# Kernel optimization log

Measured on AMD Instinct MI355X. Metric: run time of the kernel, lower is better.

Reference implementation:

```python
import jax, jax.numpy as jnp
import numpy as np

B, T, H = 32, 4096, 256
MAX_SENTS = 256  # static upper bound on sentences per doc (doc 0 has exactly 256)


def setup_inputs() -> dict:
    key = jax.random.key(0)
    hie_ins = jax.random.normal(key, (B, T, H), dtype=jnp.float32)
    # Deterministic boundary pattern: doc b has a sentence boundary (token id 1)
    # every (16 + b) tokens; all other tokens get a non-boundary id (2).
    pos = np.arange(T)
    rows = [np.where((pos + 1) % (16 + b) == 0, 1, 2) for b in range(B)]
    batch_x = jnp.asarray(np.stack(rows), dtype=jnp.int32)
    return {"hie_ins": hie_ins, "batch_x": batch_x}


def reference(hie_ins, batch_x):
    # Faithful vectorized version of HieLayer.forward with mean pooling:
    # tokens are assigned to sentence segments by exclusive cumsum of boundary
    # flags; tokens after the last boundary are dropped (as in the torch slicing
    # up to the last cut). Each sentence is mean-pooled over its true length;
    # docs are padded with zeros to MAX_SENTS sentences (== max(doc_lens)).
    _, t, _ = hie_ins.shape
    is_b = (batch_x == 1).astype(jnp.int32)          # (B, T) boundary flags
    sent_id = jnp.cumsum(is_b, axis=1) - is_b        # exclusive cumsum: sentence index per token
    doc_lens = jnp.sum(is_b, axis=1)                 # (B,) number of sentences per doc
    valid = sent_id < doc_lens[:, None]              # drop tokens past last boundary
    seg = jnp.where(valid, sent_id, MAX_SENTS)       # invalid tokens -> overflow bucket

    def per_doc(x, s):
        sums = jax.ops.segment_sum(x, s, num_segments=MAX_SENTS + 1)              # (S+1, H)
        cnts = jax.ops.segment_sum(jnp.ones((t,), x.dtype), s, num_segments=MAX_SENTS + 1)
        return sums[:MAX_SENTS], cnts[:MAX_SENTS]

    sums, cnts = jax.vmap(per_doc)(hie_ins, seg)     # (B, S, H), (B, S)
    pooled = sums / jnp.maximum(cnts, 1.0)[..., None]
    sent_valid = jnp.arange(MAX_SENTS)[None, :] < doc_lens[:, None]
    pooled = jnp.where(sent_valid[..., None], pooled, 0.0)  # zero-pad like F.pad
    return pooled, doc_lens
```

## Files before the change

### kernel.cpp

```cpp
#include <hip/hip_runtime.h>
#include <hip/hip_bf16.h>

#define NB 32
#define NT 4096
#define NH 256
#define NS 256

__global__ void hie_fused_kernel(const float* __restrict__ x,
                                 const int* __restrict__ batch_x,
                                 float* __restrict__ out) {
    const int b    = blockIdx.y;
    const int tid  = threadIdx.x;
    const int wid  = tid >> 6;
    const int lane = tid & 63;

    __shared__ int sm_w[5];
    __shared__ int sm_bpos[NS + 1];
    __shared__ int sm_len;

    const int  base = tid * 16;
    const int4* rp  = reinterpret_cast<const int4*>(batch_x + (size_t)b * NT + base);
    int flags = 0, cnt = 0;
#pragma unroll
    for (int i = 0; i < 4; ++i) {
        int4 v = rp[i];
        int f0 = (v.x == 1), f1 = (v.y == 1), f2 = (v.z == 1), f3 = (v.w == 1);
        flags |= (f0 << (4 * i)) | (f1 << (4 * i + 1)) | (f2 << (4 * i + 2)) | (f3 << (4 * i + 3));
        cnt   += f0 + f1 + f2 + f3;
    }

    int inc = cnt;
#pragma unroll
    for (int off = 1; off < 64; off <<= 1) {
        int u = __shfl_up(inc, off, 64);
        if (lane >= off) inc += u;
    }
    if (lane == 63) sm_w[wid] = inc;
    __syncthreads();
    if (tid == 0) {
        int run = 0;
#pragma unroll
        for (int w = 0; w < 4; ++w) { int t = sm_w[w]; sm_w[w] = run; run += t; }
        sm_w[4]    = run;
        sm_len     = run > NS ? NS : run;
        sm_bpos[0] = -1;
    }
    __syncthreads();

    int idx = (inc - cnt) + sm_w[wid];
#pragma unroll
    for (int i = 0; i < 16; ++i) {
        if ((flags >> i) & 1) {
            if (idx < NS) sm_bpos[idx + 1] = base + i;
            ++idx;
        }
    }
    __syncthreads();

    if (blockIdx.x == 0 && tid == 0)
        out[(size_t)NB * NS * NH + b] = (float)sm_w[4];

    const int s = blockIdx.x * 4 + wid;
    float* o = out + ((size_t)b * NS + s) * NH + lane * 4;

    if (s >= sm_len) {
        *reinterpret_cast<float4*>(o) = make_float4(0.f, 0.f, 0.f, 0.f);
        return;
    }

    const int end   = sm_bpos[s + 1];
    const int start = sm_bpos[s] + 1;
    const int n     = end - start + 1;

    const float4* p = reinterpret_cast<const float4*>(
                          x + ((size_t)b * NT + start) * NH) + lane;
    float4 a0 = make_float4(0.f, 0.f, 0.f, 0.f);
    float4 a1 = make_float4(0.f, 0.f, 0.f, 0.f);
    int k = 0;
    for (; k + 2 <= n; k += 2) {
        float4 v0 = p[0];
        float4 v1 = p[NH / 4];
        a0.x += v0.x; a0.y += v0.y; a0.z += v0.z; a0.w += v0.w;
        a1.x += v1.x; a1.y += v1.y; a1.z += v1.z; a1.w += v1.w;
        p += 2 * (NH / 4);
    }
    if (k < n) {
        float4 v0 = p[0];
        a0.x += v0.x; a0.y += v0.y; a0.z += v0.z; a0.w += v0.w;
    }
    const float inv = 1.0f / (float)n;
    *reinterpret_cast<float4*>(o) = make_float4((a0.x + a1.x) * inv,
                                                (a0.y + a1.y) * inv,
                                                (a0.z + a1.z) * inv,
                                                (a0.w + a1.w) * inv);
}

extern "C" void kernel_launch(void* const* d_in, const int* in_sizes, int n_in,
                              void* d_out, int out_size, void* d_ws, size_t ws_size,
                              hipStream_t stream) {
    const float* hie_ins = (const float*)d_in[0];
    const int*   batch_x = (const int*)d_in[1];
    float*       out     = (float*)d_out;

    hie_fused_kernel<<<dim3(NS / 4, NB), dim3(256), 0, stream>>>(hie_ins, batch_x, out);
}
```

Measured before the change: 29.45 us.

## Split boundary scan into separate kernel and pool each sentence with a full block

The fused kernel, which recomputed the boundary scan in every block, becomes two kernels. The first computes sentence boundary positions and document lengths once per document into workspace. The second pools each sentence with a 256-thread block whose four waves interleave rows and combine partial sums through shared memory. This removes redundant scan work and spreads long sentences across more waves for memory parallelism. In exchange it adds a second launch, a global round trip for the boundaries, and a shared-memory reduction.

```diff
diff --git a/kernel.cpp b/kernel.cpp
--- a/kernel.cpp
+++ b/kernel.cpp
@@ -6,17 +6,16 @@
 #define NH 256
 #define NS 256
 
-__global__ void hie_fused_kernel(const float* __restrict__ x,
-                                 const int* __restrict__ batch_x,
-                                 float* __restrict__ out) {
-    const int b    = blockIdx.y;
+__global__ void hie_scan_kernel(const int* __restrict__ batch_x,
+                                int* __restrict__ bpos,
+                                int* __restrict__ dlen,
+                                float* __restrict__ dout) {
+    const int b    = blockIdx.x;
     const int tid  = threadIdx.x;
     const int wid  = tid >> 6;
     const int lane = tid & 63;
 
     __shared__ int sm_w[5];
-    __shared__ int sm_bpos[NS + 1];
-    __shared__ int sm_len;
 
     const int  base = tid * 16;
     const int4* rp  = reinterpret_cast<const int4*>(batch_x + (size_t)b * NT + base);
@@ -41,9 +40,10 @@
         int run = 0;
 #pragma unroll
         for (int w = 0; w < 4; ++w) { int t = sm_w[w]; sm_w[w] = run; run += t; }
-        sm_w[4]    = run;
-        sm_len     = run > NS ? NS : run;
-        sm_bpos[0] = -1;
+        sm_w[4] = run;
+        bpos[b * (NS + 1)] = -1;
+        dlen[b] = run > NS ? NS : run;
+        dout[(size_t)NB * NS * NH + b] = (float)run;
     }
     __syncthreads();
 
@@ -51,48 +51,60 @@
 #pragma unroll
     for (int i = 0; i < 16; ++i) {
         if ((flags >> i) & 1) {
-            if (idx < NS) sm_bpos[idx + 1] = base + i;
+            if (idx < NS) bpos[b * (NS + 1) + 1 + idx] = base + i;
             ++idx;
         }
     }
-    __syncthreads();
+}
 
-    if (blockIdx.x == 0 && tid == 0)
-        out[(size_t)NB * NS * NH + b] = (float)sm_w[4];
+__global__ void hie_pool_kernel(const float* __restrict__ x,
+                                const int* __restrict__ bpos,
+                                const int* __restrict__ dlen,
+                                float* __restrict__ out) {
+    const int b    = blockIdx.y;
+    const int s    = blockIdx.x;
+    const int tid  = threadIdx.x;
+    const int wid  = tid >> 6;
+    const int lane = tid & 63;
 
-    const int s = blockIdx.x * 4 + wid;
-    float* o = out + ((size_t)b * NS + s) * NH + lane * 4;
+    float* orow = out + ((size_t)b * NS + s) * NH;
 
-    if (s >= sm_len) {
-        *reinterpret_cast<float4*>(o) = make_float4(0.f, 0.f, 0.f, 0.f);
+    const int L = dlen[b];
+    if (s >= L) {
+        orow[tid] = 0.0f;
         return;
     }
 
-    const int end   = sm_bpos[s + 1];
-    const int start = sm_bpos[s] + 1;
+    const int start = bpos[b * (NS + 1) + s] + 1;
+    const int end   = bpos[b * (NS + 1) + s + 1];
     const int n     = end - start + 1;
 
     const float4* p = reinterpret_cast<const float4*>(
-                          x + ((size_t)b * NT + start) * NH) + lane;
+                          x + ((size_t)b * NT + start + wid) * NH) + lane;
+    const int myrows = (n - wid + 3) >> 2;
     float4 a0 = make_float4(0.f, 0.f, 0.f, 0.f);
     float4 a1 = make_float4(0.f, 0.f, 0.f, 0.f);
     int k = 0;
-    for (; k + 2 <= n; k += 2) {
+    for (; k + 2 <= myrows; k += 2) {
         float4 v0 = p[0];
-        float4 v1 = p[NH / 4];
+        float4 v1 = p[4 * (NH / 4)];
         a0.x += v0.x; a0.y += v0.y; a0.z += v0.z; a0.w += v0.w;
         a1.x += v1.x; a1.y += v1.y; a1.z += v1.z; a1.w += v1.w;
-        p += 2 * (NH / 4);
+        p += 8 * (NH / 4);
     }
-    if (k < n) {
+    if (k < myrows) {
         float4 v0 = p[0];
         a0.x += v0.x; a0.y += v0.y; a0.z += v0.z; a0.w += v0.w;
     }
-    const float inv = 1.0f / (float)n;
-    *reinterpret_cast<float4*>(o) = make_float4((a0.x + a1.x) * inv,
-                                                (a0.y + a1.y) * inv,
-                                                (a0.z + a1.z) * inv,
-                                                (a0.w + a1.w) * inv);
+    a0.x += a1.x; a0.y += a1.y; a0.z += a1.z; a0.w += a1.w;
+
+    __shared__ float4 smp[4][64];
+    smp[wid][lane] = a0;
+    __syncthreads();
+
+    const float* smf = reinterpret_cast<const float*>(smp);
+    float v = smf[tid] + smf[256 + tid] + smf[512 + tid] + smf[768 + tid];
+    orow[tid] = v * (1.0f / (float)n);
 }
 
 extern "C" void kernel_launch(void* const* d_in, const int* in_sizes, int n_in,
@@ -102,5 +114,9 @@
     const int*   batch_x = (const int*)d_in[1];
     float*       out     = (float*)d_out;
 
-    hie_fused_kernel<<<dim3(NS / 4, NB), dim3(256), 0, stream>>>(hie_ins, batch_x, out);
+    int* bpos = (int*)d_ws;
+    int* dlen = bpos + NB * (NS + 1);
+
+    hie_scan_kernel<<<dim3(NB), dim3(256), 0, stream>>>(batch_x, bpos, dlen, out);
+    hie_pool_kernel<<<dim3(NS, NB), dim3(256), 0, stream>>>(hie_ins, bpos, dlen, out);
 }
```

New measurement: 30.61 us. 3.9% more time.
